# Optimization experiments

Hardware: AMD Instinct MI355X
Metric: run time of the kernel (lower is better)

The kernel has to match this reference:

```python
import jax, jax.numpy as jnp
import numpy as np

NUM_USERS = 1_000_000
NUM_ITEMS = 100_000
NUM_GROUPS = 500_000
EMB = 32           # forced by reshape (1, 4*32)
GROUP_SIZE = 3     # forced: 3 members + 1 item = 4 rows
B = 131_072


def setup_inputs() -> dict:
    key = jax.random.key(0)
    ks = jax.random.split(key, 12)
    return {
        "group_inputs": jax.random.randint(ks[0], (B,), 0, NUM_GROUPS),
        "item_inputs": jax.random.randint(ks[1], (B,), 0, NUM_ITEMS),
        "members": jax.random.randint(ks[2], (NUM_GROUPS, GROUP_SIZE), 0, NUM_USERS),
        "user_emb": jax.random.normal(ks[3], (NUM_USERS, EMB), jnp.float32) * 0.05,
        "item_emb": jax.random.normal(ks[4], (NUM_ITEMS, EMB - 18), jnp.float32) * 0.05,
        "genres": jax.random.uniform(ks[5], (NUM_ITEMS, 18), jnp.float32),
        "attn_W": jax.random.normal(ks[6], (4 * EMB, 3), jnp.float32) * 0.05,
        "attn_b": jax.random.normal(ks[7], (3,), jnp.float32) * 0.05,
        "pred_W1": jax.random.normal(ks[8], (3 * EMB, 8), jnp.float32) * 0.05,
        "pred_b1": jax.random.normal(ks[9], (8,), jnp.float32) * 0.05,
        "pred_W2": jax.random.normal(ks[10], (8, 1), jnp.float32) * 0.05,
        "pred_b2": jax.random.normal(ks[11], (1,), jnp.float32) * 0.05,
    }


def reference(group_inputs, item_inputs, members, user_emb, item_emb, genres,
              attn_W, attn_b, pred_W1, pred_b1, pred_W2, pred_b2):
    # item embedding: 14-d latent concat 18-d genre features -> [B, 32]
    it_e = jnp.concatenate([item_emb[item_inputs], genres[item_inputs]], axis=1)
    # members of each group -> [B, 3, 32]
    mem_e = user_emb[members[group_inputs]]
    # concat 3 member rows + 1 item row, flatten to [B, 128]
    gi = jnp.concatenate([mem_e, it_e[:, None, :]], axis=1).reshape(-1, 4 * EMB)
    # NOTE: source ConcatAttentionLayer returns the raw linear output (softmax
    # is computed but discarded), so attention "weights" are raw logits. [B, 3]
    at_wt = gi @ attn_W + attn_b
    # weighted sum of member embeddings -> [B, 32]
    g = jnp.einsum("bk,bkd->bd", at_wt, mem_e)
    new = jnp.concatenate([g * it_e, g, it_e], axis=1)  # [B, 96]
    h = jax.nn.relu(new @ pred_W1 + pred_b1)
    y = jax.nn.sigmoid(h @ pred_W2 + pred_b2)  # [B, 1]
    return y
```

## Files before the change

### kernel.cpp

```cpp
#include <hip/hip_runtime.h>
#include <math.h>

#define EMB 32

__global__ __launch_bounds__(256, 4) void bahdanau_fused(
    const int* __restrict__ group_inputs,
    const int* __restrict__ item_inputs,
    const int* __restrict__ members,
    const float* __restrict__ user_emb,
    const float* __restrict__ item_emb,
    const float* __restrict__ genres,
    const float* __restrict__ attn_W,
    const float* __restrict__ attn_b,
    const float* __restrict__ pred_W1,
    const float* __restrict__ pred_b1,
    const float* __restrict__ pred_W2,
    const float* __restrict__ pred_b2,
    float* __restrict__ out)
{
    __shared__ float s_aWT[3 * 128];
    __shared__ float s_W1T[8 * 96];
    __shared__ float s_ab[3];
    __shared__ float s_b1[8];
    __shared__ float s_W2[8];
    __shared__ float s_b2[1];

    const int tid = threadIdx.x;
    const int t = tid & 3;
    const int grp = tid >> 2;
    const int ebase = blockIdx.x * 128 + grp * 2;
    const int dbase = t * 8;

    const int2 gpair = *(const int2*)&group_inputs[ebase];
    const int2 ipair = *(const int2*)&item_inputs[ebase];

    for (int i = tid; i < 3 * 128; i += 256) {
        int k = i >> 7, d = i & 127;
        s_aWT[i] = attn_W[d * 3 + k];
    }
    for (int i = tid; i < 8 * 96; i += 256) {
        int c = i / 96, r = i - c * 96;
        s_W1T[i] = pred_W1[r * 8 + c];
    }
    if (tid < 3) s_ab[tid] = attn_b[tid];
    else if (tid < 11) s_b1[tid - 3] = pred_b1[tid - 3];
    else if (tid < 19) s_W2[tid - 11] = pred_W2[tid - 11];
    else if (tid == 19) s_b2[0] = pred_b2[0];

    __syncthreads();

    const int g0 = gpair.x, g1 = gpair.y;
    const int i0 = ipair.x, i1 = ipair.y;
    int m0[3], m1[3];
#pragma unroll
    for (int j = 0; j < 3; ++j) {
        m0[j] = members[3 * g0 + j];
        m1[j] = members[3 * g1 + j];
    }

    float itv0[8], itv1[8];
#pragma unroll
    for (int i = 0; i < 4; ++i) {
        const int d = dbase + 2 * i;
        const float2* p0 = (d < 14)
            ? (const float2*)(item_emb + (size_t)i0 * 14 + d)
            : (const float2*)(genres   + (size_t)i0 * 18 + (d - 14));
        const float2 a = *p0;
        itv0[2 * i] = a.x; itv0[2 * i + 1] = a.y;
    }
#pragma unroll
    for (int i = 0; i < 4; ++i) {
        const int d = dbase + 2 * i;
        const float2* p1 = (d < 14)
            ? (const float2*)(item_emb + (size_t)i1 * 14 + d)
            : (const float2*)(genres   + (size_t)i1 * 18 + (d - 14));
        const float2 b = *p1;
        itv1[2 * i] = b.x; itv1[2 * i + 1] = b.y;
    }

    float mem0[3][8], mem1[3][8];
#pragma unroll
    for (int j = 0; j < 3; ++j) {
        const float4* p0 = (const float4*)(user_emb + (size_t)m0[j] * EMB + dbase);
        float4 a = p0[0], b = p0[1];
        mem0[j][0] = a.x; mem0[j][1] = a.y; mem0[j][2] = a.z; mem0[j][3] = a.w;
        mem0[j][4] = b.x; mem0[j][5] = b.y; mem0[j][6] = b.z; mem0[j][7] = b.w;
    }
#pragma unroll
    for (int j = 0; j < 3; ++j) {
        const float4* p1 = (const float4*)(user_emb + (size_t)m1[j] * EMB + dbase);
        float4 c = p1[0], d = p1[1];
        mem1[j][0] = c.x; mem1[j][1] = c.y; mem1[j][2] = c.z; mem1[j][3] = c.w;
        mem1[j][4] = d.x; mem1[j][5] = d.y; mem1[j][6] = d.z; mem1[j][7] = d.w;
    }

    float hq0, hq1;
    {
        float aw[3];
#pragma unroll
        for (int k = 0; k < 3; ++k) {
            float a0 = 0.f;
#pragma unroll
            for (int j = 0; j < 3; ++j) {
                const float4* wp = (const float4*)&s_aWT[k * 128 + j * 32 + dbase];
                float4 wl = wp[0], wh = wp[1];
                float w[8] = {wl.x, wl.y, wl.z, wl.w, wh.x, wh.y, wh.z, wh.w};
#pragma unroll
                for (int i = 0; i < 8; ++i) a0 = fmaf(mem0[j][i], w[i], a0);
            }
            const float4* wp = (const float4*)&s_aWT[k * 128 + 96 + dbase];
            float4 wl = wp[0], wh = wp[1];
            float w[8] = {wl.x, wl.y, wl.z, wl.w, wh.x, wh.y, wh.z, wh.w};
#pragma unroll
            for (int i = 0; i < 8; ++i) a0 = fmaf(itv0[i], w[i], a0);
            a0 += __shfl_xor(a0, 1, 4);
            a0 += __shfl_xor(a0, 2, 4);
            aw[k] = a0 + s_ab[k];
        }
        float gv[8];
#pragma unroll
        for (int i = 0; i < 8; ++i)
            gv[i] = aw[0] * mem0[0][i] + aw[1] * mem0[1][i] + aw[2] * mem0[2][i];
        float ph[8];
#pragma unroll
        for (int c = 0; c < 8; ++c) {
            const float4* wpa = (const float4*)&s_W1T[c * 96 + dbase];
            const float4* wpb = (const float4*)&s_W1T[c * 96 + 32 + dbase];
            const float4* wpc = (const float4*)&s_W1T[c * 96 + 64 + dbase];
            float4 al = wpa[0], ah = wpa[1];
            float4 bl = wpb[0], bh = wpb[1];
            float4 cl = wpc[0], ch = wpc[1];
            float wa[8] = {al.x, al.y, al.z, al.w, ah.x, ah.y, ah.z, ah.w};
            float wb[8] = {bl.x, bl.y, bl.z, bl.w, bh.x, bh.y, bh.z, bh.w};
            float wc[8] = {cl.x, cl.y, cl.z, cl.w, ch.x, ch.y, ch.z, ch.w};
            float a0 = 0.f;
#pragma unroll
            for (int i = 0; i < 8; ++i) {
                a0 = fmaf(gv[i], fmaf(itv0[i], wa[i], wb[i]), a0);
                a0 = fmaf(itv0[i], wc[i], a0);
            }
            ph[c] = a0;
        }
        float y = s_b2[0];
#pragma unroll
        for (int c = 0; c < 8; ++c) {
            float v = ph[c];
            v += __shfl_xor(v, 1, 4);
            v += __shfl_xor(v, 2, 4);
            float h = fmaxf(v + s_b1[c], 0.0f);
            y = fmaf(h, s_W2[c], y);
        }
        hq0 = y;
    }

    {
        float aw[3];
#pragma unroll
        for (int k = 0; k < 3; ++k) {
            float a1 = 0.f;
#pragma unroll
            for (int j = 0; j < 3; ++j) {
                const float4* wp = (const float4*)&s_aWT[k * 128 + j * 32 + dbase];
                float4 wl = wp[0], wh = wp[1];
                float w[8] = {wl.x, wl.y, wl.z, wl.w, wh.x, wh.y, wh.z, wh.w};
#pragma unroll
                for (int i = 0; i < 8; ++i) a1 = fmaf(mem1[j][i], w[i], a1);
            }
            const float4* wp = (const float4*)&s_aWT[k * 128 + 96 + dbase];
            float4 wl = wp[0], wh = wp[1];
            float w[8] = {wl.x, wl.y, wl.z, wl.w, wh.x, wh.y, wh.z, wh.w};
#pragma unroll
            for (int i = 0; i < 8; ++i) a1 = fmaf(itv1[i], w[i], a1);
            a1 += __shfl_xor(a1, 1, 4);
            a1 += __shfl_xor(a1, 2, 4);
            aw[k] = a1 + s_ab[k];
        }
        float gv[8];
#pragma unroll
        for (int i = 0; i < 8; ++i)
            gv[i] = aw[0] * mem1[0][i] + aw[1] * mem1[1][i] + aw[2] * mem1[2][i];
        float ph[8];
#pragma unroll
        for (int c = 0; c < 8; ++c) {
            const float4* wpa = (const float4*)&s_W1T[c * 96 + dbase];
            const float4* wpb = (const float4*)&s_W1T[c * 96 + 32 + dbase];
            const float4* wpc = (const float4*)&s_W1T[c * 96 + 64 + dbase];
            float4 al = wpa[0], ah = wpa[1];
            float4 bl = wpb[0], bh = wpb[1];
            float4 cl = wpc[0], ch = wpc[1];
            float wa[8] = {al.x, al.y, al.z, al.w, ah.x, ah.y, ah.z, ah.w};
            float wb[8] = {bl.x, bl.y, bl.z, bl.w, bh.x, bh.y, bh.z, bh.w};
            float wc[8] = {cl.x, cl.y, cl.z, cl.w, ch.x, ch.y, ch.z, ch.w};
            float a1 = 0.f;
#pragma unroll
            for (int i = 0; i < 8; ++i) {
                a1 = fmaf(gv[i], fmaf(itv1[i], wa[i], wb[i]), a1);
                a1 = fmaf(itv1[i], wc[i], a1);
            }
            ph[c] = a1;
        }
        float y = s_b2[0];
#pragma unroll
        for (int c = 0; c < 8; ++c) {
            float v = ph[c];
            v += __shfl_xor(v, 1, 4);
            v += __shfl_xor(v, 2, 4);
            float h = fmaxf(v + s_b1[c], 0.0f);
            y = fmaf(h, s_W2[c], y);
        }
        hq1 = y;
    }

    if (t < 2) {
        float y = (t == 0) ? hq0 : hq1;
        y = 1.0f / (1.0f + expf(-y));
        out[ebase + t] = y;
    }
}

extern "C" void kernel_launch(void* const* d_in, const int* in_sizes, int n_in,
                              void* d_out, int out_size, void* d_ws, size_t ws_size,
                              hipStream_t stream) {
    const int*   group_inputs = (const int*)d_in[0];
    const int*   item_inputs  = (const int*)d_in[1];
    const int*   members      = (const int*)d_in[2];
    const float* user_emb     = (const float*)d_in[3];
    const float* item_emb     = (const float*)d_in[4];
    const float* genres       = (const float*)d_in[5];
    const float* attn_W       = (const float*)d_in[6];
    const float* attn_b       = (const float*)d_in[7];
    const float* pred_W1      = (const float*)d_in[8];
    const float* pred_b1      = (const float*)d_in[9];
    const float* pred_W2      = (const float*)d_in[10];
    const float* pred_b2      = (const float*)d_in[11];
    float* out = (float*)d_out;

    const int B = in_sizes[0];
    const int blocks = B / 128;

    bahdanau_fused<<<blocks, 256, 0, stream>>>(
        group_inputs, item_inputs, members, user_emb, item_emb, genres,
        attn_W, attn_b, pred_W1, pred_b1, pred_W2, pred_b2, out);
}
```

Before: 216.7 us.

## Process one batch row per 4-thread group and issue gathers before weight staging

Each 4-thread group now handles one batch element instead of two. The grid doubles and the launch bounds rise to 6 blocks per SM, trading per-thread memory-level parallelism for higher occupancy with fewer registers per thread. The index, member and embedding gathers are issued before the shared-memory weight staging and barrier, so their latency overlaps the weight copy. The cost is that each block now stages the shared weights for half as many elements.

```diff
diff --git a/kernel.cpp b/kernel.cpp
--- a/kernel.cpp
+++ b/kernel.cpp
@@ -3,7 +3,7 @@
 
 #define EMB 32
 
-__global__ __launch_bounds__(256, 4) void bahdanau_fused(
+__global__ __launch_bounds__(256, 6) void bahdanau_fused(
     const int* __restrict__ group_inputs,
     const int* __restrict__ item_inputs,
     const int* __restrict__ members,
@@ -28,11 +28,35 @@
     const int tid = threadIdx.x;
     const int t = tid & 3;
     const int grp = tid >> 2;
-    const int ebase = blockIdx.x * 128 + grp * 2;
+    const int e = blockIdx.x * 64 + grp;
     const int dbase = t * 8;
 
-    const int2 gpair = *(const int2*)&group_inputs[ebase];
-    const int2 ipair = *(const int2*)&item_inputs[ebase];
+    const int g0 = group_inputs[e];
+    const int i0 = item_inputs[e];
+
+    int m0[3];
+#pragma unroll
+    for (int j = 0; j < 3; ++j) m0[j] = members[3 * g0 + j];
+
+    float itv0[8];
+#pragma unroll
+    for (int i = 0; i < 4; ++i) {
+        const int d = dbase + 2 * i;
+        const float2* p0 = (d < 14)
+            ? (const float2*)(item_emb + (size_t)i0 * 14 + d)
+            : (const float2*)(genres   + (size_t)i0 * 18 + (d - 14));
+        const float2 a = *p0;
+        itv0[2 * i] = a.x; itv0[2 * i + 1] = a.y;
+    }
+
+    float mem0[3][8];
+#pragma unroll
+    for (int j = 0; j < 3; ++j) {
+        const float4* p0 = (const float4*)(user_emb + (size_t)m0[j] * EMB + dbase);
+        float4 a = p0[0], b = p0[1];
+        mem0[j][0] = a.x; mem0[j][1] = a.y; mem0[j][2] = a.z; mem0[j][3] = a.w;
+        mem0[j][4] = b.x; mem0[j][5] = b.y; mem0[j][6] = b.z; mem0[j][7] = b.w;
+    }
 
     for (int i = tid; i < 3 * 128; i += 256) {
         int k = i >> 7, d = i & 127;
@@ -46,175 +70,61 @@
     else if (tid < 11) s_b1[tid - 3] = pred_b1[tid - 3];
     else if (tid < 19) s_W2[tid - 11] = pred_W2[tid - 11];
     else if (tid == 19) s_b2[0] = pred_b2[0];
-
     __syncthreads();
 
-    const int g0 = gpair.x, g1 = gpair.y;
-    const int i0 = ipair.x, i1 = ipair.y;
-    int m0[3], m1[3];
+    float aw[3];
 #pragma unroll
-    for (int j = 0; j < 3; ++j) {
-        m0[j] = members[3 * g0 + j];
-        m1[j] = members[3 * g1 + j];
-    }
-
-    float itv0[8], itv1[8];
+    for (int k = 0; k < 3; ++k) {
+        float a0 = 0.f;
 #pragma unroll
-    for (int i = 0; i < 4; ++i) {
-        const int d = dbase + 2 * i;
-        const float2* p0 = (d < 14)
-            ? (const float2*)(item_emb + (size_t)i0 * 14 + d)
-            : (const float2*)(genres   + (size_t)i0 * 18 + (d - 14));
-        const float2 a = *p0;
-        itv0[2 * i] = a.x; itv0[2 * i + 1] = a.y;
-    }
-#pragma unroll
-    for (int i = 0; i < 4; ++i) {
-        const int d = dbase + 2 * i;
-        const float2* p1 = (d < 14)
-            ? (const float2*)(item_emb + (size_t)i1 * 14 + d)
-            : (const float2*)(genres   + (size_t)i1 * 18 + (d - 14));
-        const float2 b = *p1;
-        itv1[2 * i] = b.x; itv1[2 * i + 1] = b.y;
-    }
-
-    float mem0[3][8], mem1[3][8];
-#pragma unroll
-    for (int j = 0; j < 3; ++j) {
-        const float4* p0 = (const float4*)(user_emb + (size_t)m0[j] * EMB + dbase);
-        float4 a = p0[0], b = p0[1];
-        mem0[j][0] = a.x; mem0[j][1] = a.y; mem0[j][2] = a.z; mem0[j][3] = a.w;
-        mem0[j][4] = b.x; mem0[j][5] = b.y; mem0[j][6] = b.z; mem0[j][7] = b.w;
-    }
-#pragma unroll
-    for (int j = 0; j < 3; ++j) {
-        const float4* p1 = (const float4*)(user_emb + (size_t)m1[j] * EMB + dbase);
-        float4 c = p1[0], d = p1[1];
-        mem1[j][0] = c.x; mem1[j][1] = c.y; mem1[j][2] = c.z; mem1[j][3] = c.w;
-        mem1[j][4] = d.x; mem1[j][5] = d.y; mem1[j][6] = d.z; mem1[j][7] = d.w;
-    }
-
-    float hq0, hq1;
-    {
-        float aw[3];
-#pragma unroll
-        for (int k = 0; k < 3; ++k) {
-            float a0 = 0.f;
-#pragma unroll
-            for (int j = 0; j < 3; ++j) {
-                const float4* wp = (const float4*)&s_aWT[k * 128 + j * 32 + dbase];
-                float4 wl = wp[0], wh = wp[1];
-                float w[8] = {wl.x, wl.y, wl.z, wl.w, wh.x, wh.y, wh.z, wh.w};
-#pragma unroll
-                for (int i = 0; i < 8; ++i) a0 = fmaf(mem0[j][i], w[i], a0);
-            }
-            const float4* wp = (const float4*)&s_aWT[k * 128 + 96 + dbase];
+        for (int j = 0; j < 3; ++j) {
+            const float4* wp = (const float4*)&s_aWT[k * 128 + j * 32 + dbase];
             float4 wl = wp[0], wh = wp[1];
             float w[8] = {wl.x, wl.y, wl.z, wl.w, wh.x, wh.y, wh.z, wh.w};
 #pragma unroll
-            for (int i = 0; i < 8; ++i) a0 = fmaf(itv0[i], w[i], a0);
-            a0 += __shfl_xor(a0, 1, 4);
-            a0 += __shfl_xor(a0, 2, 4);
-            aw[k] = a0 + s_ab[k];
+            for (int i = 0; i < 8; ++i) a0 = fmaf(mem0[j][i], w[i], a0);
         }
-        float gv[8];
+        const float4* wp = (const float4*)&s_aWT[k * 128 + 96 + dbase];
+        float4 wl = wp[0], wh = wp[1];
+        float w[8] = {wl.x, wl.y, wl.z, wl.w, wh.x, wh.y, wh.z, wh.w};
 #pragma unroll
-        for (int i = 0; i < 8; ++i)
-            gv[i] = aw[0] * mem0[0][i] + aw[1] * mem0[1][i] + aw[2] * mem0[2][i];
-        float ph[8];
-#pragma unroll
-        for (int c = 0; c < 8; ++c) {
-            const float4* wpa = (const float4*)&s_W1T[c * 96 + dbase];
-            const float4* wpb = (const float4*)&s_W1T[c * 96 + 32 + dbase];
-            const float4* wpc = (const float4*)&s_W1T[c * 96 + 64 + dbase];
-            float4 al = wpa[0], ah = wpa[1];
-            float4 bl = wpb[0], bh = wpb[1];
-            float4 cl = wpc[0], ch = wpc[1];
-            float wa[8] = {al.x, al.y, al.z, al.w, ah.x, ah.y, ah.z, ah.w};
-            float wb[8] = {bl.x, bl.y, bl.z, bl.w, bh.x, bh.y, bh.z, bh.w};
-            float wc[8] = {cl.x, cl.y, cl.z, cl.w, ch.x, ch.y, ch.z, ch.w};
-            float a0 = 0.f;
-#pragma unroll
-            for (int i = 0; i < 8; ++i) {
-                a0 = fmaf(gv[i], fmaf(itv0[i], wa[i], wb[i]), a0);
-                a0 = fmaf(itv0[i], wc[i], a0);
-            }
-            ph[c] = a0;
-        }
-        float y = s_b2[0];
-#pragma unroll
-        for (int c = 0; c < 8; ++c) {
-            float v = ph[c];
-            v += __shfl_xor(v, 1, 4);
-            v += __shfl_xor(v, 2, 4);
-            float h = fmaxf(v + s_b1[c], 0.0f);
-            y = fmaf(h, s_W2[c], y);
-        }
-        hq0 = y;
+        for (int i = 0; i < 8; ++i) a0 = fmaf(itv0[i], w[i], a0);
+        a0 += __shfl_xor(a0, 1, 4);
+        a0 += __shfl_xor(a0, 2, 4);
+        aw[k] = a0 + s_ab[k];
     }
 
-    {
-        float aw[3];
+    float gv[8];
 #pragma unroll
-        for (int k = 0; k < 3; ++k) {
-            float a1 = 0.f;
+    for (int i = 0; i < 8; ++i)
+        gv[i] = aw[0] * mem0[0][i] + aw[1] * mem0[1][i] + aw[2] * mem0[2][i];
+
+    float y = s_b2[0];
 #pragma unroll
-            for (int j = 0; j < 3; ++j) {
-                const float4* wp = (const float4*)&s_aWT[k * 128 + j * 32 + dbase];
-                float4 wl = wp[0], wh = wp[1];
-                float w[8] = {wl.x, wl.y, wl.z, wl.w, wh.x, wh.y, wh.z, wh.w};
+    for (int c = 0; c < 8; ++c) {
+        const float4* wpa = (const float4*)&s_W1T[c * 96 + dbase];
+        const float4* wpb = (const float4*)&s_W1T[c * 96 + 32 + dbase];
+        const float4* wpc = (const float4*)&s_W1T[c * 96 + 64 + dbase];
+        float4 al = wpa[0], ah = wpa[1];
+        float4 bl = wpb[0], bh = wpb[1];
+        float4 cl = wpc[0], ch = wpc[1];
+        float wa[8] = {al.x, al.y, al.z, al.w, ah.x, ah.y, ah.z, ah.w};
+        float wb[8] = {bl.x, bl.y, bl.z, bl.w, bh.x, bh.y, bh.z, bh.w};
+        float wc[8] = {cl.x, cl.y, cl.z, cl.w, ch.x, ch.y, ch.z, ch.w};
+        float a0 = 0.f;
 #pragma unroll
-                for (int i = 0; i < 8; ++i) a1 = fmaf(mem1[j][i], w[i], a1);
-            }
-            const float4* wp = (const float4*)&s_aWT[k * 128 + 96 + dbase];
-            float4 wl = wp[0], wh = wp[1];
-            float w[8] = {wl.x, wl.y, wl.z, wl.w, wh.x, wh.y, wh.z, wh.w};
-#pragma unroll
-            for (int i = 0; i < 8; ++i) a1 = fmaf(itv1[i], w[i], a1);
-            a1 += __shfl_xor(a1, 1, 4);
-            a1 += __shfl_xor(a1, 2, 4);
-            aw[k] = a1 + s_ab[k];
+        for (int i = 0; i < 8; ++i) {
+            a0 = fmaf(gv[i], fmaf(itv0[i], wa[i], wb[i]), a0);
+            a0 = fmaf(itv0[i], wc[i], a0);
         }
-        float gv[8];
-#pragma unroll
-        for (int i = 0; i < 8; ++i)
-            gv[i] = aw[0] * mem1[0][i] + aw[1] * mem1[1][i] + aw[2] * mem1[2][i];
-        float ph[8];
-#pragma unroll
-        for (int c = 0; c < 8; ++c) {
-            const float4* wpa = (const float4*)&s_W1T[c * 96 + dbase];
-            const float4* wpb = (const float4*)&s_W1T[c * 96 + 32 + dbase];
-            const float4* wpc = (const float4*)&s_W1T[c * 96 + 64 + dbase];
-            float4 al = wpa[0], ah = wpa[1];
-            float4 bl = wpb[0], bh = wpb[1];
-            float4 cl = wpc[0], ch = wpc[1];
-            float wa[8] = {al.x, al.y, al.z, al.w, ah.x, ah.y, ah.z, ah.w};
-            float wb[8] = {bl.x, bl.y, bl.z, bl.w, bh.x, bh.y, bh.z, bh.w};
-            float wc[8] = {cl.x, cl.y, cl.z, cl.w, ch.x, ch.y, ch.z, ch.w};
-            float a1 = 0.f;
-#pragma unroll
-            for (int i = 0; i < 8; ++i) {
-                a1 = fmaf(gv[i], fmaf(itv1[i], wa[i], wb[i]), a1);
-                a1 = fmaf(itv1[i], wc[i], a1);
-            }
-            ph[c] = a1;
-        }
-        float y = s_b2[0];
-#pragma unroll
-        for (int c = 0; c < 8; ++c) {
-            float v = ph[c];
-            v += __shfl_xor(v, 1, 4);
-            v += __shfl_xor(v, 2, 4);
-            float h = fmaxf(v + s_b1[c], 0.0f);
-            y = fmaf(h, s_W2[c], y);
-        }
-        hq1 = y;
+        a0 += __shfl_xor(a0, 1, 4);
+        a0 += __shfl_xor(a0, 2, 4);
+        float h = fmaxf(a0 + s_b1[c], 0.0f);
+        y = fmaf(h, s_W2[c], y);
     }
 
-    if (t < 2) {
-        float y = (t == 0) ? hq0 : hq1;
-        y = 1.0f / (1.0f + expf(-y));
-        out[ebase + t] = y;
+    if (t == 0) {
+        out[e] = 1.0f / (1.0f + expf(-y));
     }
 }
 
@@ -236,7 +146,7 @@
     float* out = (float*)d_out;
 
     const int B = in_sizes[0];
-    const int blocks = B / 128;
+    const int blocks = B / 64;
 
     bahdanau_fused<<<blocks, 256, 0, stream>>>(
         group_inputs, item_inputs, members, user_emb, item_emb, genres,
```

Result: faster. 210.1 us (-3.0%).
